# Optimization experiments

Hardware: AMD Instinct MI355X
Metric: run time of the kernel (lower is better)

The kernel has to match this reference:

```python
import jax, jax.numpy as jnp
import numpy as np

N, E = 50000, 800000
D, F, H = 128, 16, 8
HD = D // H  # head_dim = 16


def setup_inputs() -> dict:
    key = jax.random.key(0)
    ks = jax.random.split(key, 9)
    s = 1.0 / np.sqrt(D)
    return {
        "x": jax.random.normal(ks[0], (N, D), dtype=jnp.float32),
        "edge_index": jax.random.randint(ks[1], (2, E), 0, N, dtype=jnp.int32),
        "edge_attr": jax.random.normal(ks[2], (E, F), dtype=jnp.float32),
        "Wq": jax.random.normal(ks[3], (D, D), dtype=jnp.float32) * s,
        "Wk": jax.random.normal(ks[4], (D, D), dtype=jnp.float32) * s,
        "Wv": jax.random.normal(ks[5], (D, D), dtype=jnp.float32) * s,
        "We": jax.random.normal(ks[6], (H, F), dtype=jnp.float32) * (1.0 / np.sqrt(F)),
        "Wo": jax.random.normal(ks[7], (D, D), dtype=jnp.float32) * s,
        "bo": jax.random.normal(ks[8], (D,), dtype=jnp.float32) * 0.01,
    }


def reference(x, edge_index, edge_attr, Wq, Wk, Wv, We, Wo, bo):
    src, tgt = edge_index[0], edge_index[1]
    # Projections, reshaped to (N, H, HD)
    Q = (x @ Wq.T).reshape(N, H, HD)
    K = (x @ Wk.T).reshape(N, H, HD)
    V = (x @ Wv.T).reshape(N, H, HD)
    # Per-edge scores: (E, H)
    attn = jnp.einsum('ehd,ehd->eh', Q[src], K[tgt]) / jnp.sqrt(jnp.float32(HD))
    attn = attn + edge_attr @ We.T  # edge bias (E, H)
    # Scatter softmax over target node segments
    m = jax.ops.segment_max(attn, tgt, num_segments=N)  # (N, H)
    m = jnp.where(jnp.isneginf(m), 0.0, m)
    e = jnp.exp(attn - m[tgt])
    ssum = jax.ops.segment_sum(e, tgt, num_segments=N)  # (N, H)
    ssum = jnp.where(ssum == 0.0, 1.0, ssum)
    a = e / ssum[tgt]  # (E, H); dropout p=0.0 -> identity
    # Weighted scatter-add aggregation: (N, D)
    out_edge = (a[:, :, None] * V[tgt]).reshape(E, D)
    out = jnp.zeros((N, D), dtype=x.dtype).at[tgt].add(out_edge)
    return out @ Wo.T + bo
```

## Files before the change

### kernel.cpp

```cpp
#include <hip/hip_runtime.h>
#include <hip/hip_bf16.h>

#define NN 50000
#define NE 800000
#define DD 128
#define MARK_BLOCKS 782


typedef __bf16 bf16x8 __attribute__((ext_vector_type(8)));
typedef float floatx4 __attribute__((ext_vector_type(4)));

__global__ __launch_bounds__(256) void prep_kernel(
        const int* __restrict__ tgt,
        const float* __restrict__ Wo,
        const float* __restrict__ Wv,
        unsigned char* __restrict__ mask,
        __hip_bfloat16* __restrict__ Wc) {
    const int b = blockIdx.x;
    if (b < MARK_BLOCKS) {
        int i4 = b * 256 + threadIdx.x;
        if (i4 < NE / 4) {
            int4 t = reinterpret_cast<const int4*>(tgt)[i4];
            mask[t.x] = 1; mask[t.y] = 1; mask[t.z] = 1; mask[t.w] = 1;
        }
    } else {
        int idx = (b - MARK_BLOCKS) * 256 + threadIdx.x;
        int j = idx >> 7, k = idx & 127;
        float acc = 0.f;
#pragma unroll 8
        for (int t = 0; t < DD; ++t)
            acc += Wo[j * DD + t] * Wv[t * DD + k];
        Wc[idx] = __float2bfloat16(acc);
    }
}

#define LDSW (DD + 8)

__global__ __launch_bounds__(512) void final_gemm_kernel(
        const float* __restrict__ x,
        const __hip_bfloat16* __restrict__ Wc,
        const unsigned char* __restrict__ mask,
        const float* __restrict__ bo,
        float* __restrict__ out) {
    __shared__ __hip_bfloat16 sWc[DD * LDSW];

    const int tid = threadIdx.x;

    for (int it = 0; it < 4; ++it) {
        int chunk = it * 512 + tid;
        int row = chunk >> 4;
        int c = chunk & 15;
        uint4 v = *reinterpret_cast<const uint4*>(Wc + row * DD + c * 8);
        *reinterpret_cast<uint4*>(&sWc[row * LDSW + c * 8]) = v;
    }
    __syncthreads();

    const int wave = tid >> 6;
    const int lane = tid & 63;
    const int l15 = lane & 15;
    const int quad = lane >> 4;
    const long rowBase = (long)blockIdx.x * 128 + wave * 16;

    floatx4 acc[8];
#pragma unroll
    for (int nf = 0; nf < 8; ++nf) acc[nf] = (floatx4){0.f, 0.f, 0.f, 0.f};

    long arow = rowBase + l15;
    if (arow > NN - 1) arow = NN - 1;
    const float* xrow = x + arow * DD;
#pragma unroll
    for (int ks = 0; ks < 4; ++ks) {
        const int kOff = ks * 32 + quad * 8;
        floatx4 lo = *reinterpret_cast<const floatx4*>(xrow + kOff);
        floatx4 hi = *reinterpret_cast<const floatx4*>(xrow + kOff + 4);
        bf16x8 afrag;
#pragma unroll
        for (int j = 0; j < 4; ++j) { afrag[j] = (__bf16)lo[j]; afrag[4 + j] = (__bf16)hi[j]; }
#pragma unroll
        for (int nf = 0; nf < 8; ++nf) {
            const bf16x8 bfrag = *reinterpret_cast<const bf16x8*>(
                &sWc[(nf * 16 + l15) * LDSW + kOff]);
            acc[nf] = __builtin_amdgcn_mfma_f32_16x16x32_bf16(afrag, bfrag, acc[nf], 0, 0, 0);
        }
    }

    float bov[8];
#pragma unroll
    for (int nf = 0; nf < 8; ++nf) bov[nf] = bo[nf * 16 + l15];

#pragma unroll
    for (int r = 0; r < 4; ++r) {
        long grow = rowBase + quad * 4 + r;
        if (grow < NN) {
            float mv = (mask[grow] == 1) ? 1.0f : 0.0f;
#pragma unroll
            for (int nf = 0; nf < 8; ++nf) {
                out[grow * DD + nf * 16 + l15] = acc[nf][r] * mv + bov[nf];
            }
        }
    }
}

extern "C" void kernel_launch(void* const* d_in, const int* in_sizes, int n_in,
                              void* d_out, int out_size, void* d_ws, size_t ws_size,
                              hipStream_t stream) {
    const float* x        = (const float*)d_in[0];
    const int* edge_index = (const int*)d_in[1];
    const float* Wv       = (const float*)d_in[5];
    const float* Wo       = (const float*)d_in[7];
    const float* bo       = (const float*)d_in[8];
    float* out = (float*)d_out;

    unsigned char* mask = (unsigned char*)d_ws;
    __hip_bfloat16* Wc  = (__hip_bfloat16*)((char*)d_ws + 50176);

    prep_kernel<<<MARK_BLOCKS + 64, 256, 0, stream>>>(edge_index + NE, Wo, Wv, mask, Wc);
    final_gemm_kernel<<<(NN + 127) / 128, 512, 0, stream>>>(x, Wc, mask, bo, out);
}
```

Before: 129.2 us.

## Fuse mask/Wc prep and GEMM into one cooperative kernel with grid sync

The separate prep kernel (target-mask marking plus the Wo·Wv product) and the output GEMM kernel are merged into one cooperative kernel. A grid-wide sync separates the two phases. This removes one kernel launch and the gap between dependent launches. In exchange it adds a grid barrier and requires all 391 blocks to be co-resident. If the cooperative launch fails, it falls back to the original two launches.

```diff
diff --git a/kernel.cpp b/kernel.cpp
--- a/kernel.cpp
+++ b/kernel.cpp
@@ -1,51 +1,50 @@
 #include <hip/hip_runtime.h>
 #include <hip/hip_bf16.h>
+#include <hip/hip_cooperative_groups.h>
+
+namespace cg = cooperative_groups;
 
 #define NN 50000
 #define NE 800000
 #define DD 128
+#define GBLOCKS 391
 #define MARK_BLOCKS 782
 
 
 typedef __bf16 bf16x8 __attribute__((ext_vector_type(8)));
 typedef float floatx4 __attribute__((ext_vector_type(4)));
 
-__global__ __launch_bounds__(256) void prep_kernel(
-        const int* __restrict__ tgt,
-        const float* __restrict__ Wo,
-        const float* __restrict__ Wv,
-        unsigned char* __restrict__ mask,
-        __hip_bfloat16* __restrict__ Wc) {
-    const int b = blockIdx.x;
-    if (b < MARK_BLOCKS) {
-        int i4 = b * 256 + threadIdx.x;
-        if (i4 < NE / 4) {
-            int4 t = reinterpret_cast<const int4*>(tgt)[i4];
-            mask[t.x] = 1; mask[t.y] = 1; mask[t.z] = 1; mask[t.w] = 1;
-        }
-    } else {
-        int idx = (b - MARK_BLOCKS) * 256 + threadIdx.x;
-        int j = idx >> 7, k = idx & 127;
-        float acc = 0.f;
-#pragma unroll 8
-        for (int t = 0; t < DD; ++t)
-            acc += Wo[j * DD + t] * Wv[t * DD + k];
-        Wc[idx] = __float2bfloat16(acc);
+#define LDSW (DD + 8)
+
+
+__device__ __forceinline__ void do_mark(const int* __restrict__ tgt,
+                                        unsigned char* __restrict__ mask,
+                                        int i4) {
+    if (i4 < NE / 4) {
+        int4 t = reinterpret_cast<const int4*>(tgt)[i4];
+        mask[t.x] = 1; mask[t.y] = 1; mask[t.z] = 1; mask[t.w] = 1;
     }
 }
 
-#define LDSW (DD + 8)
+__device__ __forceinline__ void do_wc(const float* __restrict__ Wo,
+                                      const float* __restrict__ Wv,
+                                      __hip_bfloat16* __restrict__ Wc,
+                                      int idx) {
+    int j = idx >> 7, k = idx & 127;
+    float acc = 0.f;
+#pragma unroll 8
+    for (int t = 0; t < DD; ++t)
+        acc += Wo[j * DD + t] * Wv[t * DD + k];
+    Wc[idx] = __float2bfloat16(acc);
+}
 
-__global__ __launch_bounds__(512) void final_gemm_kernel(
-        const float* __restrict__ x,
-        const __hip_bfloat16* __restrict__ Wc,
-        const unsigned char* __restrict__ mask,
-        const float* __restrict__ bo,
-        float* __restrict__ out) {
-    __shared__ __hip_bfloat16 sWc[DD * LDSW];
-
-    const int tid = threadIdx.x;
-
+__device__ __forceinline__ void do_gemm_tile(const float* __restrict__ x,
+                                             const __hip_bfloat16* __restrict__ Wc,
+                                             const unsigned char* __restrict__ mask,
+                                             const float* __restrict__ bo,
+                                             float* __restrict__ out,
+                                             __hip_bfloat16* sWc,
+                                             int b, int tid) {
     for (int it = 0; it < 4; ++it) {
         int chunk = it * 512 + tid;
         int row = chunk >> 4;
@@ -59,7 +58,7 @@
     const int lane = tid & 63;
     const int l15 = lane & 15;
     const int quad = lane >> 4;
-    const long rowBase = (long)blockIdx.x * 128 + wave * 16;
+    const long rowBase = (long)b * 128 + wave * 16;
 
     floatx4 acc[8];
 #pragma unroll
@@ -101,6 +100,53 @@
     }
 }
 
+
+__global__ __launch_bounds__(512) void fused_kernel(
+        const float* __restrict__ x,
+        const int* __restrict__ tgt,
+        const float* __restrict__ Wo,
+        const float* __restrict__ Wv,
+        const float* __restrict__ bo,
+        unsigned char* __restrict__ mask,
+        __hip_bfloat16* __restrict__ Wc,
+        float* __restrict__ out) {
+    __shared__ __hip_bfloat16 sWc[DD * LDSW];
+    const int tid = threadIdx.x;
+    const int b = blockIdx.x;
+
+    do_mark(tgt, mask, b * 512 + tid);
+    if (b < 64 && tid < 256) do_wc(Wo, Wv, Wc, b * 256 + tid);
+
+    cg::this_grid().sync();
+
+    do_gemm_tile(x, Wc, mask, bo, out, sWc, b, tid);
+}
+
+
+__global__ __launch_bounds__(256) void prep_kernel(
+        const int* __restrict__ tgt,
+        const float* __restrict__ Wo,
+        const float* __restrict__ Wv,
+        unsigned char* __restrict__ mask,
+        __hip_bfloat16* __restrict__ Wc) {
+    const int b = blockIdx.x;
+    if (b < MARK_BLOCKS) {
+        do_mark(tgt, mask, b * 256 + threadIdx.x);
+    } else {
+        do_wc(Wo, Wv, Wc, (b - MARK_BLOCKS) * 256 + threadIdx.x);
+    }
+}
+
+__global__ __launch_bounds__(512) void final_gemm_kernel(
+        const float* __restrict__ x,
+        const __hip_bfloat16* __restrict__ Wc,
+        const unsigned char* __restrict__ mask,
+        const float* __restrict__ bo,
+        float* __restrict__ out) {
+    __shared__ __hip_bfloat16 sWc[DD * LDSW];
+    do_gemm_tile(x, Wc, mask, bo, out, sWc, blockIdx.x, threadIdx.x);
+}
+
 extern "C" void kernel_launch(void* const* d_in, const int* in_sizes, int n_in,
                               void* d_out, int out_size, void* d_ws, size_t ws_size,
                               hipStream_t stream) {
@@ -114,6 +160,13 @@
     unsigned char* mask = (unsigned char*)d_ws;
     __hip_bfloat16* Wc  = (__hip_bfloat16*)((char*)d_ws + 50176);
 
-    prep_kernel<<<MARK_BLOCKS + 64, 256, 0, stream>>>(edge_index + NE, Wo, Wv, mask, Wc);
-    final_gemm_kernel<<<(NN + 127) / 128, 512, 0, stream>>>(x, Wc, mask, bo, out);
+    const int* tgt = edge_index + NE;
+    void* args[] = {(void*)&x, (void*)&tgt, (void*)&Wo, (void*)&Wv,
+                    (void*)&bo, (void*)&mask, (void*)&Wc, (void*)&out};
+    hipError_t e = hipLaunchCooperativeKernel((void*)fused_kernel, dim3(GBLOCKS),
+                                              dim3(512), args, 0, stream);
+    if (e != hipSuccess) {
+        prep_kernel<<<MARK_BLOCKS + 64, 256, 0, stream>>>(tgt, Wo, Wv, mask, Wc);
+        final_gemm_kernel<<<GBLOCKS, 512, 0, stream>>>(x, Wc, mask, bo, out);
+    }
 }
```

Measured after the change: 198.9 us. 53.9% more time.
